# Optimization experiments

Hardware: AMD Instinct MI355X
Metric: run time of the kernel (lower is better)

## Reference

```python
import jax, jax.numpy as jnp
import numpy as np

H = 16  # n_head

def _rms_norm(x):
    eps = jnp.asarray(jnp.finfo(x.dtype).eps, x.dtype)
    ms = jnp.mean(jnp.square(x), axis=-1, keepdims=True)
    return x * jax.lax.rsqrt(ms + eps)

def _interp(x, pos):
    # x: [B,T,H,Dh]; pos: [B,T,H,Dh] float positions along axis 1
    T = x.shape[1]
    pos_floor = jnp.floor(pos)
    pos0 = jnp.clip(pos_floor, 0, T - 1).astype(jnp.int32)
    pos1 = jnp.clip(pos0 + 1, 0, T - 1)
    frac = pos - pos_floor
    x0 = jnp.take_along_axis(x, pos0, axis=1)
    x1 = jnp.take_along_axis(x, pos1, axis=1)
    return x0 + (x1 - x0) * frac

def setup_inputs() -> dict:
    key = jax.random.key(0)
    ks = jax.random.split(key, 5)
    B, T, D = 4, 4096, 2048
    x = jax.random.normal(ks[0], (B, T, D), dtype=jnp.float32)
    scale = 0.02
    Wq = jax.random.normal(ks[1], (D, D), dtype=jnp.float32) * scale
    Wk = jax.random.normal(ks[2], (D, D), dtype=jnp.float32) * scale
    Wsq = jax.random.normal(ks[3], (D, D), dtype=jnp.float32) * scale
    Wsk = jax.random.normal(ks[4], (D, D), dtype=jnp.float32) * scale
    return {"x": x, "Wq": Wq, "Wk": Wk, "Wsq": Wsq, "Wsk": Wsk}

def reference(x, Wq, Wk, Wsq, Wsk):
    B, T, D = x.shape
    Dh = D // H
    # projections (Linear with weight [out,in]: y = x @ W.T)
    q = _rms_norm((x @ Wq.T).reshape(B, T, H, Dh))
    k = _rms_norm((x @ Wk.T).reshape(B, T, H, Dh))
    sq = jax.nn.softplus(x @ Wsq.T).reshape(B, T, H, Dh)
    sk = jax.nn.softplus(x @ Wsk.T).reshape(B, T, H, Dh)
    t_idx = jnp.arange(T, dtype=x.dtype).reshape(1, T, 1, 1)
    posq = jnp.minimum(jnp.maximum(t_idx - sq, 0.0), t_idx)
    posk = jnp.minimum(jnp.maximum(t_idx - sk, 0.0), t_idx)
    q_def = _interp(q, posq)
    k_def = _interp(k, posk)
    return (q_def * k_def).reshape(B, T, D)
```

## Files before the change

kernel.cpp:

```cpp
#include <hip/hip_runtime.h>

typedef unsigned short u16;
typedef __bf16 bf16x8 __attribute__((ext_vector_type(8)));
typedef unsigned short u16x8 __attribute__((ext_vector_type(8)));
typedef unsigned short u16x4 __attribute__((ext_vector_type(4)));
typedef float f32x4 __attribute__((ext_vector_type(4)));

#define K_DIM 2048
#define BM 128
#define BN 128
#define BK 32

#define GLL16(g, l) __builtin_amdgcn_global_load_lds( \
    (const __attribute__((address_space(1))) void*)(g), \
    (__attribute__((address_space(3))) void*)(l), 16, 0, 0)

__device__ __forceinline__ u16 f2bf(float f) {
    unsigned int u = __builtin_bit_cast(unsigned int, f);
    u = (u + 0x7fffu + ((u >> 16) & 1u)) >> 16;
    return (u16)u;
}
__device__ __forceinline__ float bf2f(u16 h) {
    unsigned int u = ((unsigned int)h) << 16;
    return __builtin_bit_cast(float, u);
}
__device__ __forceinline__ float softplus_f(float v) {
    return fmaxf(v, 0.0f) + log1pf(expf(-fabsf(v)));
}

__global__ void pack_kernel(const float* __restrict__ src, u16* __restrict__ dst, int n4) {
    int i = blockIdx.x * blockDim.x + threadIdx.x;
    if (i >= n4) return;
    float4 v = ((const float4*)src)[i];
    u16x4 o;
    o[0] = f2bf(v.x); o[1] = f2bf(v.y); o[2] = f2bf(v.z); o[3] = f2bf(v.w);
    ((u16x4*)dst)[i] = o;
}

__global__ __launch_bounds__(256) void gemm_fused(
    const u16* __restrict__ xb, const u16* __restrict__ wb,
    u16* __restrict__ qb, u16* __restrict__ kb,
    u16* __restrict__ sqb, u16* __restrict__ skb)
{
    __shared__ u16 Als[BM * BK];
    __shared__ u16 Bls[BM * BK];
    __shared__ float ss[BM];

    const int tid  = threadIdx.x;
    const int lane = tid & 63;
    const int wave = tid >> 6;
    const int wm = wave >> 1;
    const int wn = wave & 1;
    const int gm0 = blockIdx.y * BM;
    const int gn0 = blockIdx.x * BN;

    const int r0 = tid >> 2;
    const int qs = ((tid & 3) - ((tid >> 3) & 3)) & 3;
    const int kc = qs * 8;
    const u16* gA0 = xb + (size_t)(gm0 + r0) * K_DIM + kc;
    const u16* gA1 = gA0 + (size_t)64 * K_DIM;
    const u16* gB0 = wb + (size_t)(gn0 + r0) * K_DIM + kc;
    const u16* gB1 = gB0 + (size_t)64 * K_DIM;
    char* lA0 = (char*)Als + wave * 1024;
    char* lA1 = (char*)Als + 4096 + wave * 1024;
    char* lB0 = (char*)Bls + wave * 1024;
    char* lB1 = (char*)Bls + 4096 + wave * 1024;

    f32x4 acc[4][4] = {};

    const int mr = lane & 15;
    const int q  = lane >> 4;
    const int s  = (q + (mr >> 1)) & 3;
    const int fragoff = mr * 32 + s * 8;

    for (int kt = 0; kt < K_DIM / BK; ++kt) {
        GLL16(gA0, lA0); GLL16(gA1, lA1);
        GLL16(gB0, lB0); GLL16(gB1, lB1);
        gA0 += BK; gA1 += BK; gB0 += BK; gB1 += BK;
        __syncthreads();

        bf16x8 a[4], b[4];
#pragma unroll
        for (int i = 0; i < 4; ++i)
            a[i] = __builtin_bit_cast(bf16x8, *(const u16x8*)&Als[(wm * 4 + i) * 512 + fragoff]);
#pragma unroll
        for (int j = 0; j < 4; ++j)
            b[j] = __builtin_bit_cast(bf16x8, *(const u16x8*)&Bls[(wn * 4 + j) * 512 + fragoff]);
#pragma unroll
        for (int i = 0; i < 4; ++i)
#pragma unroll
            for (int j = 0; j < 4; ++j)
                acc[i][j] = __builtin_amdgcn_mfma_f32_16x16x32_bf16(a[i], b[j], acc[i][j], 0, 0, 0);
        __syncthreads();
    }

    const int which = gn0 >> 11;
    if (tid < BM) ss[tid] = 0.0f;
    __syncthreads();

    const int mbase = wm * 64 + (lane >> 4) * 4;
    const int col0  = (gn0 & 2047) + wn * 64 + (lane & 15);

    if (which < 2) {
#pragma unroll
        for (int i = 0; i < 4; ++i) {
#pragma unroll
            for (int r = 0; r < 4; ++r) {
                float sv = acc[i][0][r] * acc[i][0][r] + acc[i][1][r] * acc[i][1][r]
                         + acc[i][2][r] * acc[i][2][r] + acc[i][3][r] * acc[i][3][r];
                sv += __shfl_xor(sv, 1, 64);
                sv += __shfl_xor(sv, 2, 64);
                sv += __shfl_xor(sv, 4, 64);
                sv += __shfl_xor(sv, 8, 64);
                if ((lane & 15) == 0) atomicAdd(&ss[mbase + i * 16 + r], sv);
            }
        }
        __syncthreads();
    }

    u16* ob = (which == 0) ? qb : (which == 1) ? kb : (which == 2) ? sqb : skb;
#pragma unroll
    for (int i = 0; i < 4; ++i) {
#pragma unroll
        for (int r = 0; r < 4; ++r) {
            int m = mbase + i * 16 + r;
            size_t rowbase = (size_t)(gm0 + m) * 2048;
            float scale = 1.0f;
            if (which < 2)
                scale = rsqrtf(ss[m] * (1.0f / 128.0f) + 1.1920929e-07f);
#pragma unroll
            for (int j = 0; j < 4; ++j) {
                float v = acc[i][j][r];
                v = (which < 2) ? v * scale : softplus_f(v);
                ob[rowbase + col0 + j * 16] = f2bf(v);
            }
        }
    }
}

__global__ void interp_mul(const u16* __restrict__ qb, const u16* __restrict__ kb,
                           const u16* __restrict__ sqb, const u16* __restrict__ skb,
                           float* __restrict__ out)
{
    size_t idx = (size_t)blockIdx.x * 256 + threadIdx.x;
    int c = (int)(idx & 2047);
    size_t bt = idx >> 11;
    int t = (int)(bt & 4095);
    float tf = (float)t;

    float sqv = bf2f(sqb[idx]);
    float skv = bf2f(skb[idx]);
    float pq = fminf(fmaxf(tf - sqv, 0.0f), tf);
    float pk = fminf(fmaxf(tf - skv, 0.0f), tf);
    float pqf = floorf(pq), pkf = floorf(pk);
    int q0i = (int)pqf, k0i = (int)pkf;
    int q1i = min(q0i + 1, 4095), k1i = min(k0i + 1, 4095);
    float fq = pq - pqf, fk = pk - pkf;

    size_t rb = (idx >> 23) << 23;
    size_t o = rb + (size_t)c;
    float q0 = bf2f(qb[o + ((size_t)q0i << 11)]);
    float q1 = bf2f(qb[o + ((size_t)q1i << 11)]);
    float k0 = bf2f(kb[o + ((size_t)k0i << 11)]);
    float k1 = bf2f(kb[o + ((size_t)k1i << 11)]);
    float qd = q0 + (q1 - q0) * fq;
    float kd = k0 + (k1 - k0) * fk;
    out[idx] = qd * kd;
}

extern "C" void kernel_launch(void* const* d_in, const int* in_sizes, int n_in,
                              void* d_out, int out_size, void* d_ws, size_t ws_size,
                              hipStream_t stream) {
    const float* x   = (const float*)d_in[0];
    const float* Wq  = (const float*)d_in[1];
    const float* Wk  = (const float*)d_in[2];
    const float* Wsq = (const float*)d_in[3];
    const float* Wsk = (const float*)d_in[4];
    float* out = (float*)d_out;

    const size_t NEED = 369098752;
    if (ws_size < NEED) return;
    char* ws = (char*)d_ws;
    u16* xb  = (u16*)(ws);
    u16* wb  = (u16*)(ws + 67108864);
    u16* qb  = (u16*)(ws + 100663296);
    u16* kb  = (u16*)(ws + 167772160);
    u16* sqb = (u16*)(ws + 234881024);
    u16* skb = (u16*)(ws + 301989888);

    pack_kernel<<<32768, 256, 0, stream>>>(x,   xb, 8388608);
    pack_kernel<<<4096,  256, 0, stream>>>(Wq,  wb,            1048576);
    pack_kernel<<<4096,  256, 0, stream>>>(Wk,  wb + 4194304,  1048576);
    pack_kernel<<<4096,  256, 0, stream>>>(Wsq, wb + 8388608,  1048576);
    pack_kernel<<<4096,  256, 0, stream>>>(Wsk, wb + 12582912, 1048576);

    dim3 ggrid(64, 128);
    gemm_fused<<<ggrid, 256, 0, stream>>>(xb, wb, qb, kb, sqb, skb);

    interp_mul<<<131072, 256, 0, stream>>>(qb, kb, sqb, skb, out);
}
```

Baseline: 1.178 ms.

## Rewrite fused GEMM as 256x256 tile with double-buffered LDS and phased MFMA schedule

The projection GEMM moves from 128x128 tiles with 4 waves and a single LDS buffer to 256x256 tiles with 8 waves, BK=64 and double-buffered LDS. Global-to-LDS loads for the next stage are interleaved with MFMA phases, separated by explicit barriers, vmcnt waits and s_setprio, so memory latency is hidden behind compute. The larger tile raises data reuse per load, and the RMS-norm reduction indexing is adapted so each 128-column head half keeps its own partial sums. The cost is high LDS use (128 KB per block) and register pressure from 32 accumulators, plus fragile hand-placed synchronisation.

```diff
diff --git a/kernel.cpp b/kernel.cpp
--- a/kernel.cpp
+++ b/kernel.cpp
@@ -7,13 +7,14 @@
 typedef float f32x4 __attribute__((ext_vector_type(4)));
 
 #define K_DIM 2048
-#define BM 128
-#define BN 128
-#define BK 32
 
 #define GLL16(g, l) __builtin_amdgcn_global_load_lds( \
     (const __attribute__((address_space(1))) void*)(g), \
     (__attribute__((address_space(3))) void*)(l), 16, 0, 0)
+
+#define PHB() do { asm volatile("" ::: "memory"); __builtin_amdgcn_s_barrier(); asm volatile("" ::: "memory"); } while (0)
+#define VMW(n) asm volatile("s_waitcnt vmcnt(" #n ")" ::: "memory")
+#define MFMA_(av, bv, cc) (cc) = __builtin_amdgcn_mfma_f32_16x16x32_bf16((av), (bv), (cc), 0, 0, 0)
 
 __device__ __forceinline__ u16 f2bf(float f) {
     unsigned int u = __builtin_bit_cast(unsigned int, f);
@@ -37,73 +38,184 @@
     ((u16x4*)dst)[i] = o;
 }
 
-__global__ __launch_bounds__(256) void gemm_fused(
+__global__ __launch_bounds__(512, 2) void gemm_fused(
     const u16* __restrict__ xb, const u16* __restrict__ wb,
     u16* __restrict__ qb, u16* __restrict__ kb,
     u16* __restrict__ sqb, u16* __restrict__ skb)
 {
-    __shared__ u16 Als[BM * BK];
-    __shared__ u16 Bls[BM * BK];
-    __shared__ float ss[BM];
+    __shared__ __align__(16) u16 Als[32768];
+    __shared__ __align__(16) u16 Bls[32768];
+    __shared__ float ss[512];
 
     const int tid  = threadIdx.x;
     const int lane = tid & 63;
     const int wave = tid >> 6;
-    const int wm = wave >> 1;
-    const int wn = wave & 1;
-    const int gm0 = blockIdx.y * BM;
-    const int gn0 = blockIdx.x * BN;
-
-    const int r0 = tid >> 2;
-    const int qs = ((tid & 3) - ((tid >> 3) & 3)) & 3;
-    const int kc = qs * 8;
-    const u16* gA0 = xb + (size_t)(gm0 + r0) * K_DIM + kc;
-    const u16* gA1 = gA0 + (size_t)64 * K_DIM;
-    const u16* gB0 = wb + (size_t)(gn0 + r0) * K_DIM + kc;
-    const u16* gB1 = gB0 + (size_t)64 * K_DIM;
-    char* lA0 = (char*)Als + wave * 1024;
-    char* lA1 = (char*)Als + 4096 + wave * 1024;
-    char* lB0 = (char*)Bls + wave * 1024;
-    char* lB1 = (char*)Bls + 4096 + wave * 1024;
-
-    f32x4 acc[4][4] = {};
-
-    const int mr = lane & 15;
-    const int q  = lane >> 4;
-    const int s  = (q + (mr >> 1)) & 3;
-    const int fragoff = mr * 32 + s * 8;
-
-    for (int kt = 0; kt < K_DIM / BK; ++kt) {
-        GLL16(gA0, lA0); GLL16(gA1, lA1);
-        GLL16(gB0, lB0); GLL16(gB1, lB1);
-        gA0 += BK; gA1 += BK; gB0 += BK; gB1 += BK;
-        __syncthreads();
-
-        bf16x8 a[4], b[4];
-#pragma unroll
-        for (int i = 0; i < 4; ++i)
-            a[i] = __builtin_bit_cast(bf16x8, *(const u16x8*)&Als[(wm * 4 + i) * 512 + fragoff]);
-#pragma unroll
-        for (int j = 0; j < 4; ++j)
-            b[j] = __builtin_bit_cast(bf16x8, *(const u16x8*)&Bls[(wn * 4 + j) * 512 + fragoff]);
-#pragma unroll
-        for (int i = 0; i < 4; ++i)
-#pragma unroll
-            for (int j = 0; j < 4; ++j)
-                acc[i][j] = __builtin_amdgcn_mfma_f32_16x16x32_bf16(a[i], b[j], acc[i][j], 0, 0, 0);
-        __syncthreads();
+    const int wm   = wave >> 2;
+    const int wn   = wave & 3;
+    const int gm0  = blockIdx.y * 256;
+    const int gn0  = blockIdx.x * 256;
+
+    const int q8 = (((lane & 3) - ((lane >> 3) & 3)) & 3) * 8;
+    int offS[4]; const u16* pa[4]; const u16* pb[4];
+#pragma unroll
+    for (int l = 0; l < 4; ++l) {
+        const int G = l * 8 + wave;
+        const int s = G >> 4, g = G & 15;
+        offS[l] = s * 8192 + g * 512;
+        const int r = g * 16 + (lane >> 2);
+        pa[l] = xb + (size_t)(gm0 + r) * K_DIM + s * 32 + q8;
+        pb[l] = wb + (size_t)(gn0 + r) * K_DIM + s * 32 + q8;
     }
 
+    const int mr  = lane & 15;
+    const int srd = ((lane >> 4) + (mr >> 1)) & 3;
+    const int fro = mr * 32 + srd * 8;
+    const int aRB = wm * 8 * 512 + fro;
+    const int bRB = wn * 4 * 512 + fro;
+
+    f32x4 acc[8][4] = {};
+
+#pragma unroll
+    for (int l = 0; l < 4; ++l) GLL16(pa[l], &Als[offS[l]]);
+#pragma unroll
+    for (int l = 0; l < 4; ++l) GLL16(pb[l], &Bls[offS[l]]);
+#pragma unroll
+    for (int l = 0; l < 4; ++l) GLL16(pb[l] + 64, &Bls[16384 + offS[l]]);
+    __syncthreads();
+
+#define LDA(buf, i, ks) __builtin_bit_cast(bf16x8, *(const u16x8*)&Als[(buf)*16384 + (ks)*8192 + aRB + (i)*512])
+#define LDB(buf, j, ks) __builtin_bit_cast(bf16x8, *(const u16x8*)&Bls[(buf)*16384 + (ks)*8192 + bRB + (j)*512])
+
+    for (int it = 0; it < 16; ++it) {
+        bf16x8 a03[4][2], a47[4][2], b01[2][2], b23[2][2];
+
+#pragma unroll
+        for (int i = 0; i < 4; ++i) { a03[i][0] = LDA(0, i, 0); a03[i][1] = LDA(0, i, 1); }
+#pragma unroll
+        for (int j = 0; j < 2; ++j) { b01[j][0] = LDB(0, j, 0); b01[j][1] = LDB(0, j, 1); }
+        GLL16(pa[0] + 64, &Als[16384 + offS[0]]);
+        GLL16(pa[1] + 64, &Als[16384 + offS[1]]);
+        PHB();
+        __builtin_amdgcn_s_setprio(1);
+#pragma unroll
+        for (int i = 0; i < 4; ++i) {
+            MFMA_(a03[i][0], b01[0][0], acc[i][0]); MFMA_(a03[i][1], b01[0][1], acc[i][0]);
+            MFMA_(a03[i][0], b01[1][0], acc[i][1]); MFMA_(a03[i][1], b01[1][1], acc[i][1]);
+        }
+        __builtin_amdgcn_s_setprio(0);
+        PHB();
+
+#pragma unroll
+        for (int j = 0; j < 2; ++j) { b23[j][0] = LDB(0, j + 2, 0); b23[j][1] = LDB(0, j + 2, 1); }
+        GLL16(pa[2] + 64, &Als[16384 + offS[2]]);
+        GLL16(pa[3] + 64, &Als[16384 + offS[3]]);
+        PHB();
+        __builtin_amdgcn_s_setprio(1);
+#pragma unroll
+        for (int i = 0; i < 4; ++i) {
+            MFMA_(a03[i][0], b23[0][0], acc[i][2]); MFMA_(a03[i][1], b23[0][1], acc[i][2]);
+            MFMA_(a03[i][0], b23[1][0], acc[i][3]); MFMA_(a03[i][1], b23[1][1], acc[i][3]);
+        }
+        __builtin_amdgcn_s_setprio(0);
+        PHB();
+
+#pragma unroll
+        for (int i = 0; i < 4; ++i) { a47[i][0] = LDA(0, i + 4, 0); a47[i][1] = LDA(0, i + 4, 1); }
+        GLL16(pb[0] + 128, &Bls[offS[0]]);
+        GLL16(pb[1] + 128, &Bls[offS[1]]);
+        PHB();
+        __builtin_amdgcn_s_setprio(1);
+#pragma unroll
+        for (int i = 0; i < 4; ++i) {
+            MFMA_(a47[i][0], b23[0][0], acc[4 + i][2]); MFMA_(a47[i][1], b23[0][1], acc[4 + i][2]);
+            MFMA_(a47[i][0], b23[1][0], acc[4 + i][3]); MFMA_(a47[i][1], b23[1][1], acc[4 + i][3]);
+        }
+        __builtin_amdgcn_s_setprio(0);
+        PHB();
+
+        GLL16(pb[2] + 128, &Bls[offS[2]]);
+        GLL16(pb[3] + 128, &Bls[offS[3]]);
+        PHB();
+        __builtin_amdgcn_s_setprio(1);
+#pragma unroll
+        for (int i = 0; i < 4; ++i) {
+            MFMA_(a47[i][0], b01[0][0], acc[4 + i][0]); MFMA_(a47[i][1], b01[0][1], acc[4 + i][0]);
+            MFMA_(a47[i][0], b01[1][0], acc[4 + i][1]); MFMA_(a47[i][1], b01[1][1], acc[4 + i][1]);
+        }
+        __builtin_amdgcn_s_setprio(0);
+        VMW(4);
+        PHB();
+
+#pragma unroll
+        for (int i = 0; i < 4; ++i) { a03[i][0] = LDA(1, i, 0); a03[i][1] = LDA(1, i, 1); }
+#pragma unroll
+        for (int j = 0; j < 2; ++j) { b01[j][0] = LDB(1, j, 0); b01[j][1] = LDB(1, j, 1); }
+        GLL16(pa[0] + 128, &Als[offS[0]]);
+        GLL16(pa[1] + 128, &Als[offS[1]]);
+        PHB();
+        __builtin_amdgcn_s_setprio(1);
+#pragma unroll
+        for (int i = 0; i < 4; ++i) {
+            MFMA_(a03[i][0], b01[0][0], acc[i][0]); MFMA_(a03[i][1], b01[0][1], acc[i][0]);
+            MFMA_(a03[i][0], b01[1][0], acc[i][1]); MFMA_(a03[i][1], b01[1][1], acc[i][1]);
+        }
+        __builtin_amdgcn_s_setprio(0);
+        PHB();
+
+#pragma unroll
+        for (int j = 0; j < 2; ++j) { b23[j][0] = LDB(1, j + 2, 0); b23[j][1] = LDB(1, j + 2, 1); }
+        GLL16(pa[2] + 128, &Als[offS[2]]);
+        GLL16(pa[3] + 128, &Als[offS[3]]);
+        PHB();
+        __builtin_amdgcn_s_setprio(1);
+#pragma unroll
+        for (int i = 0; i < 4; ++i) {
+            MFMA_(a03[i][0], b23[0][0], acc[i][2]); MFMA_(a03[i][1], b23[0][1], acc[i][2]);
+            MFMA_(a03[i][0], b23[1][0], acc[i][3]); MFMA_(a03[i][1], b23[1][1], acc[i][3]);
+        }
+        __builtin_amdgcn_s_setprio(0);
+        PHB();
+
+#pragma unroll
+        for (int i = 0; i < 4; ++i) { a47[i][0] = LDA(1, i + 4, 0); a47[i][1] = LDA(1, i + 4, 1); }
+        GLL16(pb[0] + 192, &Bls[16384 + offS[0]]);
+        GLL16(pb[1] + 192, &Bls[16384 + offS[1]]);
+        PHB();
+        __builtin_amdgcn_s_setprio(1);
+#pragma unroll
+        for (int i = 0; i < 4; ++i) {
+            MFMA_(a47[i][0], b23[0][0], acc[4 + i][2]); MFMA_(a47[i][1], b23[0][1], acc[4 + i][2]);
+            MFMA_(a47[i][0], b23[1][0], acc[4 + i][3]); MFMA_(a47[i][1], b23[1][1], acc[4 + i][3]);
+        }
+        __builtin_amdgcn_s_setprio(0);
+        PHB();
+
+        GLL16(pb[2] + 192, &Bls[16384 + offS[2]]);
+        GLL16(pb[3] + 192, &Bls[16384 + offS[3]]);
+        PHB();
+        __builtin_amdgcn_s_setprio(1);
+#pragma unroll
+        for (int i = 0; i < 4; ++i) {
+            MFMA_(a47[i][0], b01[0][0], acc[4 + i][0]); MFMA_(a47[i][1], b01[0][1], acc[4 + i][0]);
+            MFMA_(a47[i][0], b01[1][0], acc[4 + i][1]); MFMA_(a47[i][1], b01[1][1], acc[4 + i][1]);
+        }
+        __builtin_amdgcn_s_setprio(0);
+        VMW(4);
+        PHB();
+
+#pragma unroll
+        for (int l = 0; l < 4; ++l) { pa[l] += 128; pb[l] += 128; }
+    }
+    VMW(0);
+
     const int which = gn0 >> 11;
-    if (tid < BM) ss[tid] = 0.0f;
+    ss[tid] = 0.0f;
     __syncthreads();
 
-    const int mbase = wm * 64 + (lane >> 4) * 4;
-    const int col0  = (gn0 & 2047) + wn * 64 + (lane & 15);
-
+    const int h = wn >> 1;
     if (which < 2) {
 #pragma unroll
-        for (int i = 0; i < 4; ++i) {
+        for (int i = 0; i < 8; ++i) {
 #pragma unroll
             for (int r = 0; r < 4; ++r) {
                 float sv = acc[i][0][r] * acc[i][0][r] + acc[i][1][r] * acc[i][1][r]
@@ -112,22 +224,24 @@
                 sv += __shfl_xor(sv, 2, 64);
                 sv += __shfl_xor(sv, 4, 64);
                 sv += __shfl_xor(sv, 8, 64);
-                if ((lane & 15) == 0) atomicAdd(&ss[mbase + i * 16 + r], sv);
+                if ((lane & 15) == 0)
+                    atomicAdd(&ss[h * 256 + wm * 128 + i * 16 + (lane >> 4) * 4 + r], sv);
             }
         }
         __syncthreads();
     }
 
     u16* ob = (which == 0) ? qb : (which == 1) ? kb : (which == 2) ? sqb : skb;
-#pragma unroll
-    for (int i = 0; i < 4; ++i) {
+    const int col0 = (gn0 & 2047) + wn * 64 + (lane & 15);
+#pragma unroll
+    for (int i = 0; i < 8; ++i) {
 #pragma unroll
         for (int r = 0; r < 4; ++r) {
-            int m = mbase + i * 16 + r;
-            size_t rowbase = (size_t)(gm0 + m) * 2048;
+            const int m = wm * 128 + i * 16 + (lane >> 4) * 4 + r;
+            const size_t rowbase = (size_t)(gm0 + m) * 2048;
             float scale = 1.0f;
             if (which < 2)
-                scale = rsqrtf(ss[m] * (1.0f / 128.0f) + 1.1920929e-07f);
+                scale = rsqrtf(ss[h * 256 + m] * (1.0f / 128.0f) + 1.1920929e-07f);
 #pragma unroll
             for (int j = 0; j < 4; ++j) {
                 float v = acc[i][j][r];
@@ -194,8 +308,8 @@
     pack_kernel<<<4096,  256, 0, stream>>>(Wsq, wb + 8388608,  1048576);
     pack_kernel<<<4096,  256, 0, stream>>>(Wsk, wb + 12582912, 1048576);
 
-    dim3 ggrid(64, 128);
-    gemm_fused<<<ggrid, 256, 0, stream>>>(xb, wb, qb, kb, sqb, skb);
+    dim3 ggrid(32, 64);
+    gemm_fused<<<ggrid, 512, 0, stream>>>(xb, wb, qb, kb, sqb, skb);
 
     interp_mul<<<131072, 256, 0, stream>>>(qb, kb, sqb, skb, out);
 }
```

Result: slower. 1.472 ms (+25.0%).
